# Kernel optimization log

Hardware: AMD Instinct MI355X
Metric: run time of the kernel (lower is better)

The kernel has to match this reference:

```python
import jax, jax.numpy as jnp
import numpy as np

N_GROUPS = 32
EPS = 1e-5
N_HEADS = 4
D_K = 64


def group_norm(x, gamma, beta):
    # x: [B, C, H, W]; normalize over (channels within group, spatial)
    B, C, H, W = x.shape
    xg = x.reshape(B, N_GROUPS, C // N_GROUPS, H, W)
    mean = jnp.mean(xg, axis=(2, 3, 4), keepdims=True)
    var = jnp.var(xg, axis=(2, 3, 4), keepdims=True)
    xn = ((xg - mean) * jax.lax.rsqrt(var + EPS)).reshape(B, C, H, W)
    return xn * gamma[None, :, None, None] + beta[None, :, None, None]


def setup_inputs() -> dict:
    key = jax.random.key(0)
    ks = jax.random.split(key, 4)
    B, C, H, W = 4, 256, 64, 64
    x = jax.random.normal(ks[0], (B, C, H, W), dtype=jnp.float32)
    gamma = jnp.ones((C,), dtype=jnp.float32)
    beta = jnp.zeros((C,), dtype=jnp.float32)
    w_qkv = jax.random.normal(ks[1], (C, N_HEADS * D_K * 3), dtype=jnp.float32) * (C ** -0.5)
    b_qkv = jnp.zeros((N_HEADS * D_K * 3,), dtype=jnp.float32)
    w_out = jax.random.normal(ks[2], (N_HEADS * D_K, C), dtype=jnp.float32) * ((N_HEADS * D_K) ** -0.5)
    b_out = jnp.zeros((C,), dtype=jnp.float32)
    return {"x": x, "gamma": gamma, "beta": beta, "w_qkv": w_qkv,
            "b_qkv": b_qkv, "w_out": w_out, "b_out": b_out}


def reference(x, gamma, beta, w_qkv, b_qkv, w_out, b_out):
    B, C, H, W = x.shape
    S = H * W
    scale = D_K ** -0.5
    # GroupNorm -> [B, S, C]
    h = group_norm(x, gamma, beta).reshape(B, C, S).transpose(0, 2, 1)
    qkv = (h @ w_qkv + b_qkv).reshape(B, S, N_HEADS, 3 * D_K)
    q, k, v = jnp.split(qkv, 3, axis=-1)          # each [B, S, H, D]
    attn = jnp.einsum('bihd,bjhd->bijh', q, k) * scale
    attn = jax.nn.softmax(attn, axis=2)           # softmax over j (keys)
    res = jnp.einsum('bijh,bjhd->bihd', attn, v)  # [B, S, H, D]
    res = res.reshape(B, S, N_HEADS * D_K)
    res = res @ w_out + b_out                     # [B, S, C]
    res = res.transpose(0, 2, 1).reshape(B, C, H, W)
    return res + x
```

## Files before the change

### kernel.cpp

```cpp
#include <hip/hip_runtime.h>
#include <hip/hip_bf16.h>


typedef __attribute__((ext_vector_type(8))) short short8;
typedef __attribute__((ext_vector_type(4))) float f32x4;
typedef __attribute__((ext_vector_type(16))) float f32x16;

__device__ __forceinline__ unsigned short f2bf(float f) {
    union { float f; unsigned u; } v; v.f = f;
    unsigned r = v.u + 0x7FFF + ((v.u >> 16) & 1);
    return (unsigned short)(r >> 16);
}

__device__ __forceinline__ unsigned cvt_pk_bf16(float lo, float hi) {
    unsigned r;
    asm("v_cvt_pk_bf16_f32 %0, %1, %2" : "=v"(r) : "v"(lo), "v"(hi));
    return r;
}

__device__ __forceinline__ void permswap(unsigned &x, unsigned &y) {
    asm("v_permlane32_swap_b32 %0, %1" : "+v"(x), "+v"(y));
}

__device__ __forceinline__ float fexp2(float x) {
    float r;
    asm("v_exp_f32 %0, %1" : "=v"(r) : "v"(x));
    return r;
}

__device__ __forceinline__ void gl_lds16(const void* g, void* l) {
    __builtin_amdgcn_global_load_lds(
        (const __attribute__((address_space(1))) void*)(g),
        (__attribute__((address_space(3))) void*)(l), 16, 0, 0);
}

__device__ __forceinline__ f32x16 fzero16() {
    f32x16 z;
    #pragma unroll
    for (int i = 0; i < 16; ++i) z[i] = 0.f;
    return z;
}

__global__ __launch_bounds__(1024) void k_gn_stats(const float* __restrict__ x,
                                                   float* __restrict__ stats) {
    int bg = blockIdx.x;
    const float4* xp = (const float4*)(x + bg * 32768);
    float s1 = 0.f, s2 = 0.f;
    for (int i = threadIdx.x; i < 8192; i += 1024) {
        float4 v = xp[i];
        s1 += v.x + v.y + v.z + v.w;
        s2 += v.x*v.x + v.y*v.y + v.z*v.z + v.w*v.w;
    }
    #pragma unroll
    for (int off = 32; off; off >>= 1) {
        s1 += __shfl_down(s1, off);
        s2 += __shfl_down(s2, off);
    }
    __shared__ float r1[16], r2[16];
    int wid = threadIdx.x >> 6;
    if ((threadIdx.x & 63) == 0) { r1[wid] = s1; r2[wid] = s2; }
    __syncthreads();
    if (threadIdx.x == 0) {
        float a = 0.f, b = 0.f;
        #pragma unroll
        for (int i = 0; i < 16; ++i) { a += r1[i]; b += r2[i]; }
        float mean = a * (1.f/32768.f);
        float var  = b * (1.f/32768.f) - mean*mean;
        stats[bg*2]   = mean;
        stats[bg*2+1] = rsqrtf(var + 1e-5f);
    }
}

__global__ void k_cvt_w(const float* __restrict__ wqkv, const float* __restrict__ wout,
                        unsigned short* __restrict__ wqkvT, unsigned short* __restrict__ woutT) {
    int i = blockIdx.x * 256 + threadIdx.x;
    if (i < 196608) {
        int k = i / 768, n = i - k * 768;
        wqkvT[n*256 + k] = f2bf(wqkv[i]);
    }
    if (i < 65536) {
        int k = i >> 8, n = i & 255;
        woutT[n*256 + k] = f2bf(wout[i]);
    }
}

__global__ __launch_bounds__(256) void k_gn_norm(
    const float* __restrict__ x, const float* __restrict__ gamma,
    const float* __restrict__ beta, const float* __restrict__ stats,
    unsigned short* __restrict__ h) {
    __shared__ unsigned short t[64][72];
    int s0 = blockIdx.x * 64, c0 = blockIdx.y * 64, b = blockIdx.z;
    int tid = threadIdx.x;
    int sl = (tid & 15) * 4;
    int cr = tid >> 4;
    #pragma unroll
    for (int p = 0; p < 4; ++p) {
        int c = c0 + cr + p * 16;
        float4 v = *(const float4*)&x[(b*256 + c)*4096 + s0 + sl];
        int sg = (b*32 + (c >> 3)) * 2;
        float mean = stats[sg], rstd = stats[sg+1];
        float sa = rstd * gamma[c];
        float sb = beta[c] - mean * sa;
        ushort4 pk;
        pk.x = f2bf(v.x*sa + sb); pk.y = f2bf(v.y*sa + sb);
        pk.z = f2bf(v.z*sa + sb); pk.w = f2bf(v.w*sa + sb);
        *(ushort4*)&t[cr + p*16][sl] = pk;
    }
    __syncthreads();
    int sr = tid >> 2;
    int cc = (tid & 3) * 16;
    unsigned rr[8];
    #pragma unroll
    for (int j = 0; j < 8; ++j)
        rr[j] = (unsigned)t[cc + 2*j][sr] | ((unsigned)t[cc + 2*j + 1][sr] << 16);
    unsigned short* hp = &h[(b*4096 + s0 + sr)*256 + c0];
    *(uint4*)&hp[cc]     = make_uint4(rr[0], rr[1], rr[2], rr[3]);
    *(uint4*)&hp[cc + 8] = make_uint4(rr[4], rr[5], rr[6], rr[7]);
}

__global__ __launch_bounds__(256) void k_qkv(
    const unsigned short* __restrict__ h, const unsigned short* __restrict__ wT,
    const float* __restrict__ bqkv,
    unsigned short* __restrict__ q, unsigned short* __restrict__ kk,
    unsigned short* __restrict__ vT) {
    int mt = blockIdx.x, head = blockIdx.y;
    int tid = threadIdx.x;
    int wid = tid >> 6, lane = tid & 63;
    int g = lane >> 4, li = lane & 15;
    int m0 = mt * 64 + wid * 16;
    int row = m0 + li;
    f32x4 acc[12];
    #pragma unroll
    for (int nt = 0; nt < 12; ++nt) acc[nt] = (f32x4){0.f,0.f,0.f,0.f};
    #pragma unroll
    for (int kt = 0; kt < 8; ++kt) {
        short8 a = *(const short8*)&h[row*256 + kt*32 + g*8];
        #pragma unroll
        for (int nt = 0; nt < 12; ++nt) {
            int n = head*192 + nt*16 + li;
            short8 b = *(const short8*)&wT[n*256 + kt*32 + g*8];
            acc[nt] = __builtin_amdgcn_mfma_f32_16x16x32_bf16(a, b, acc[nt], 0, 0, 0);
        }
    }
    int b = m0 >> 12;
    int s0 = m0 & 4095;
    int bh = b*4 + head;
    #pragma unroll
    for (int nt = 0; nt < 12; ++nt) {
        int ng = head*192 + nt*16 + li;
        float bias = bqkv[ng];
        int d = (nt & 3)*16 + li;
        if ((nt >> 2) == 2) {
            ushort4 pk;
            pk.x = f2bf(acc[nt][0] + bias); pk.y = f2bf(acc[nt][1] + bias);
            pk.z = f2bf(acc[nt][2] + bias); pk.w = f2bf(acc[nt][3] + bias);
            *(ushort4*)&vT[(bh*64 + d)*4096 + s0 + g*4] = pk;
        } else if ((nt >> 2) == 0) {
            #pragma unroll
            for (int r = 0; r < 4; ++r)
                q[(bh*4096 + s0 + g*4 + r)*64 + d] = f2bf((acc[nt][r] + bias) * 0.1803368801f);
        } else {
            #pragma unroll
            for (int r = 0; r < 4; ++r)
                kk[(bh*4096 + s0 + g*4 + r)*64 + d] = f2bf(acc[nt][r] + bias);
        }
    }
}

__global__ __launch_bounds__(512, 4) void k_attn(
    const unsigned short* __restrict__ q, const unsigned short* __restrict__ kk,
    const unsigned short* __restrict__ vT, unsigned short* __restrict__ ao) {
    __shared__ __align__(16) char smem[65536];

    int n = blockIdx.x;
    int qt = n >> 4;
    int bh = ((n & 7) << 1) | ((n >> 3) & 1);
    int tid = threadIdx.x;
    int wid = tid >> 6, lane = tid & 63;
    int qw = wid & 3, st = wid >> 2;
    int hi = lane >> 5, il = lane & 31;
    int swl = (il & 7) << 4;

    int qbase = qt * 128 + qw * 32;
    int qrow = bh * 4096 + qbase + il;
    short8 bq[4];
    #pragma unroll
    for (int kc = 0; kc < 4; ++kc)
        bq[kc] = *(const short8*)&q[qrow*64 + kc*16 + hi*8];

    unsigned p16  = tid * 16;
    unsigned row0 = p16 >> 7;
    unsigned sw   = (row0 & 7) << 4;
    unsigned ks0  = p16 ^ sw;
    unsigned vc0  = (p16 & 127u) ^ sw;
    const char* kbase = (const char*)kk + (size_t)bh * 524288;
    const char* vbase = (const char*)vT + (size_t)(bh*64 + row0) * 8192;
    unsigned woff = wid * 1024;

#define STAGE_PAIR(d, pair) do {                                             \
    const char* _k0 = kbase + (size_t)(2*(pair)) * 8192;                     \
    size_t _vo = (size_t)(2*(pair)) * 128;                                   \
    gl_lds16(_k0 + ks0,              smem + ((d)*2+0)*8192 + woff);          \
    gl_lds16(_k0 + 8192 + ks0,       smem + ((d)*2+1)*8192 + woff);          \
    gl_lds16(vbase + _vo + vc0,       smem + 32768 + ((d)*2+0)*8192 + woff); \
    gl_lds16(vbase + _vo + 128 + vc0, smem + 32768 + ((d)*2+1)*8192 + woff); \
} while (0)

    f32x16 o0 = fzero16(), o1 = fzero16();
    float m_run = -1e30f, l_loc = 0.f;

    STAGE_PAIR(0, 0);
    asm volatile("s_waitcnt vmcnt(0)" ::: "memory");
    __builtin_amdgcn_s_barrier();
    asm volatile("" ::: "memory");

    int cur = 0;
    for (int tp = 0; tp < 32; ++tp) {
        if (tp < 31) STAGE_PAIR(cur ^ 1, tp + 1);

        const char* kb = smem + (cur*2 + st) * 8192;
        const char* vb = smem + 32768 + (cur*2 + st) * 8192;

        f32x16 s0 = fzero16(), s1 = fzero16();
        __builtin_amdgcn_s_setprio(1);
        #pragma unroll
        for (int kc = 0; kc < 4; ++kc) {
            int c = (kc*32 + hi*16) ^ swl;
            short8 ka0 = *(const short8*)(kb + il*128 + c);
            short8 ka1 = *(const short8*)(kb + 4096 + il*128 + c);
            s0 = __builtin_amdgcn_mfma_f32_32x32x16_bf16(ka0, bq[kc], s0, 0, 0, 0);
            s1 = __builtin_amdgcn_mfma_f32_32x32x16_bf16(ka1, bq[kc], s1, 0, 0, 0);
        }
        __builtin_amdgcn_s_setprio(0);

        float m8[8];
        #pragma unroll
        for (int r = 0; r < 8; ++r)
            m8[r] = fmaxf(fmaxf(s0[2*r], s0[2*r+1]), fmaxf(s1[2*r], s1[2*r+1]));
        float mx = fmaxf(fmaxf(fmaxf(m8[0], m8[1]), fmaxf(m8[2], m8[3])),
                         fmaxf(fmaxf(m8[4], m8[5]), fmaxf(m8[6], m8[7])));
        mx = fmaxf(mx, __shfl_xor(mx, 32));
        if (__any(mx > m_run)) {
            float m_new = fmaxf(m_run, mx);
            float fac = fexp2(m_run - m_new);
            l_loc *= fac;
            #pragma unroll
            for (int r = 0; r < 16; ++r) { o0[r] *= fac; o1[r] *= fac; }
            m_run = m_new;
        }
        float p0[16], p1[16];
        #pragma unroll
        for (int r = 0; r < 16; ++r) {
            p0[r] = fexp2(s0[r] - m_run);
            p1[r] = fexp2(s1[r] - m_run);
        }
        float a8[8];
        #pragma unroll
        for (int r = 0; r < 8; ++r)
            a8[r] = (p0[2*r] + p0[2*r+1]) + (p1[2*r] + p1[2*r+1]);
        float ps = ((a8[0] + a8[1]) + (a8[2] + a8[3])) + ((a8[4] + a8[5]) + (a8[6] + a8[7]));
        l_loc += ps;

        unsigned w[16];
        #pragma unroll
        for (int t = 0; t < 2; ++t) {
            const float* pp = t ? p1 : p0;
            #pragma unroll
            for (int hh = 0; hh < 2; ++hh) {
                unsigned a = cvt_pk_bf16(pp[hh*8+0], pp[hh*8+1]);
                unsigned b = cvt_pk_bf16(pp[hh*8+2], pp[hh*8+3]);
                unsigned c = cvt_pk_bf16(pp[hh*8+4], pp[hh*8+5]);
                unsigned d = cvt_pk_bf16(pp[hh*8+6], pp[hh*8+7]);
                permswap(a, c);
                permswap(b, d);
                int base = (t*2 + hh) * 4;
                w[base+0] = a; w[base+1] = b; w[base+2] = c; w[base+3] = d;
            }
        }

        __builtin_amdgcn_s_setprio(1);
        #pragma unroll
        for (int jc = 0; jc < 4; ++jc) {
            union { unsigned u[4]; short8 s8; } pb;
            pb.u[0] = w[jc*4+0]; pb.u[1] = w[jc*4+1];
            pb.u[2] = w[jc*4+2]; pb.u[3] = w[jc*4+3];
            int c = (jc*32 + hi*16) ^ swl;
            short8 va0 = *(const short8*)(vb + il*128 + c);
            short8 va1 = *(const short8*)(vb + 4096 + il*128 + c);
            o0 = __builtin_amdgcn_mfma_f32_32x32x16_bf16(va0, pb.s8, o0, 0, 0, 0);
            o1 = __builtin_amdgcn_mfma_f32_32x32x16_bf16(va1, pb.s8, o1, 0, 0, 0);
        }
        __builtin_amdgcn_s_setprio(0);

        if (tp < 31) asm volatile("s_waitcnt vmcnt(0)" ::: "memory");
        asm volatile("" ::: "memory");
        __builtin_amdgcn_s_barrier();
        asm volatile("" ::: "memory");
        cur ^= 1;
    }
#undef STAGE_PAIR

    l_loc += __shfl_xor(l_loc, 32);

    float* red = (float*)smem;
    int slot = ((qw*64 + lane) * 34);
    if (st == 1) {
        #pragma unroll
        for (int r = 0; r < 16; ++r) { red[slot + r] = o0[r]; red[slot + 16 + r] = o1[r]; }
        red[slot + 32] = l_loc;
        red[slot + 33] = m_run;
    }
    __syncthreads();
    if (st == 0) {
        float m1 = red[slot + 33], l1 = red[slot + 32];
        float m = fmaxf(m_run, m1);
        float f0 = fexp2(m_run - m), f1 = fexp2(m1 - m);
        float inv = 1.f / (l_loc * f0 + l1 * f1);
        float a0 = f0 * inv, a1 = f1 * inv;
        int b = bh >> 2, hh = bh & 3;
        int s = qbase + il;
        unsigned short* aop = &ao[((size_t)(b*4096 + s))*256 + hh*64];
        #pragma unroll
        for (int rr = 0; rr < 4; ++rr) {
            ushort4 pk0, pk1;
            pk0.x = f2bf(o0[rr*4+0]*a0 + red[slot + rr*4+0]*a1);
            pk0.y = f2bf(o0[rr*4+1]*a0 + red[slot + rr*4+1]*a1);
            pk0.z = f2bf(o0[rr*4+2]*a0 + red[slot + rr*4+2]*a1);
            pk0.w = f2bf(o0[rr*4+3]*a0 + red[slot + rr*4+3]*a1);
            *(ushort4*)&aop[rr*8 + hi*4] = pk0;
            pk1.x = f2bf(o1[rr*4+0]*a0 + red[slot + 16 + rr*4+0]*a1);
            pk1.y = f2bf(o1[rr*4+1]*a0 + red[slot + 16 + rr*4+1]*a1);
            pk1.z = f2bf(o1[rr*4+2]*a0 + red[slot + 16 + rr*4+2]*a1);
            pk1.w = f2bf(o1[rr*4+3]*a0 + red[slot + 16 + rr*4+3]*a1);
            *(ushort4*)&aop[32 + rr*8 + hi*4] = pk1;
        }
    }
}

__global__ __launch_bounds__(256) void k_out(
    const unsigned short* __restrict__ ao, const unsigned short* __restrict__ wT,
    const float* __restrict__ bout, const float* __restrict__ x,
    float* __restrict__ out) {
    int mt = blockIdx.x;
    int tid = threadIdx.x;
    int wid = tid >> 6, lane = tid & 63;
    int g = lane >> 4, li = lane & 15;
    int rg = wid & 1, ch = wid >> 1;
    int m0 = mt * 32 + rg * 16;
    int row = m0 + li;
    f32x4 acc[8];
    #pragma unroll
    for (int nt = 0; nt < 8; ++nt) acc[nt] = (f32x4){0.f,0.f,0.f,0.f};
    #pragma unroll
    for (int kt = 0; kt < 8; ++kt) {
        short8 a = *(const short8*)&ao[row*256 + kt*32 + g*8];
        #pragma unroll
        for (int nt = 0; nt < 8; ++nt) {
            int nn = ch*128 + nt*16 + li;
            short8 b = *(const short8*)&wT[nn*256 + kt*32 + g*8];
            acc[nt] = __builtin_amdgcn_mfma_f32_16x16x32_bf16(a, b, acc[nt], 0, 0, 0);
        }
    }
    int b = m0 >> 12;
    int s0 = (m0 & 4095) + g*4;
    #pragma unroll
    for (int nt = 0; nt < 8; ++nt) {
        int c = ch*128 + nt*16 + li;
        float bias = bout[c];
        int base = (b*256 + c)*4096 + s0;
        float4 xr = *(const float4*)&x[base];
        float4 ov;
        ov.x = acc[nt][0] + bias + xr.x;
        ov.y = acc[nt][1] + bias + xr.y;
        ov.z = acc[nt][2] + bias + xr.z;
        ov.w = acc[nt][3] + bias + xr.w;
        *(float4*)&out[base] = ov;
    }
}

extern "C" void kernel_launch(void* const* d_in, const int* in_sizes, int n_in,
                              void* d_out, int out_size, void* d_ws, size_t ws_size,
                              hipStream_t stream) {
    (void)in_sizes; (void)n_in; (void)out_size; (void)ws_size;
    const float* x     = (const float*)d_in[0];
    const float* gamma = (const float*)d_in[1];
    const float* beta  = (const float*)d_in[2];
    const float* wqkv  = (const float*)d_in[3];
    const float* bqkv  = (const float*)d_in[4];
    const float* wout  = (const float*)d_in[5];
    const float* bout  = (const float*)d_in[6];
    float* out = (float*)d_out;

    char* ws = (char*)d_ws;
    unsigned short* h     = (unsigned short*)(ws);
    unsigned short* q     = (unsigned short*)(ws + (8u<<20));
    unsigned short* kk    = (unsigned short*)(ws + (16u<<20));
    unsigned short* vT    = (unsigned short*)(ws + (24u<<20));
    unsigned short* ao    = (unsigned short*)(ws + (32u<<20));
    unsigned short* wqkvT = (unsigned short*)(ws + (40u<<20));
    unsigned short* woutT = (unsigned short*)(ws + (40u<<20) + 393216);
    float*          stats = (float*)(ws + (40u<<20) + 524288);

    k_gn_stats<<<128, 1024, 0, stream>>>(x, stats);
    k_cvt_w<<<768, 256, 0, stream>>>(wqkv, wout, wqkvT, woutT);
    k_gn_norm<<<dim3(64, 4, 4), 256, 0, stream>>>(x, gamma, beta, stats, h);
    k_qkv<<<dim3(256, 4), 256, 0, stream>>>(h, wqkvT, bqkv, q, kk, vT);
    k_attn<<<dim3(512), 512, 0, stream>>>(q, kk, vT, ao);
    k_out<<<dim3(512), 256, 0, stream>>>(ao, woutT, bout, x, out);
}
```

Measured before the change: 180.5 us.

## Fold max subtraction into MFMA init and compute row sums via ones-MFMA

Seeds the QK^T accumulators with -m_run so the max subtraction happens inside the MFMA, exponentiates first, and rescales only when a probability exceeds a threshold (lazy rescale in the exp domain with log2 tracking). The row-sum reduction is replaced by an extra MFMA against a ones matrix that accumulates l alongside the PV product, and bf16 packing is interleaved into the PV loop. This trims VALU work (subtracts, sum tree, shuffle) in the softmax but adds a third MFMA per step and a log2/reciprocal on the rescale path. It also risks precision, since l is accumulated from bf16-rounded probabilities and the threshold lets exponentials grow before rescaling.

```diff
diff --git a/kernel.cpp b/kernel.cpp
--- a/kernel.cpp
+++ b/kernel.cpp
@@ -188,6 +188,10 @@
     for (int kc = 0; kc < 4; ++kc)
         bq[kc] = *(const short8*)&q[qrow*64 + kc*16 + hi*8];
 
+    short8 ones;
+    #pragma unroll
+    for (int i = 0; i < 8; ++i) ones[i] = (short)0x3F80;
+
     unsigned p16  = tid * 16;
     unsigned row0 = p16 >> 7;
     unsigned sw   = (row0 & 7) << 4;
@@ -206,8 +210,8 @@
     gl_lds16(vbase + _vo + 128 + vc0, smem + 32768 + ((d)*2+1)*8192 + woff); \
 } while (0)
 
-    f32x16 o0 = fzero16(), o1 = fzero16();
-    float m_run = -1e30f, l_loc = 0.f;
+    f32x16 o0 = fzero16(), o1 = fzero16(), accl = fzero16();
+    float m_run = 0.f;
 
     STAGE_PAIR(0, 0);
     asm volatile("s_waitcnt vmcnt(0)" ::: "memory");
@@ -221,74 +225,70 @@
         const char* kb = smem + (cur*2 + st) * 8192;
         const char* vb = smem + 32768 + (cur*2 + st) * 8192;
 
-        f32x16 s0 = fzero16(), s1 = fzero16();
+        float nm = -m_run;
+        f32x16 p0, p1;
+        #pragma unroll
+        for (int r = 0; r < 16; ++r) { p0[r] = nm; p1[r] = nm; }
         __builtin_amdgcn_s_setprio(1);
         #pragma unroll
         for (int kc = 0; kc < 4; ++kc) {
             int c = (kc*32 + hi*16) ^ swl;
             short8 ka0 = *(const short8*)(kb + il*128 + c);
             short8 ka1 = *(const short8*)(kb + 4096 + il*128 + c);
-            s0 = __builtin_amdgcn_mfma_f32_32x32x16_bf16(ka0, bq[kc], s0, 0, 0, 0);
-            s1 = __builtin_amdgcn_mfma_f32_32x32x16_bf16(ka1, bq[kc], s1, 0, 0, 0);
+            p0 = __builtin_amdgcn_mfma_f32_32x32x16_bf16(ka0, bq[kc], p0, 0, 0, 0);
+            p1 = __builtin_amdgcn_mfma_f32_32x32x16_bf16(ka1, bq[kc], p1, 0, 0, 0);
         }
         __builtin_amdgcn_s_setprio(0);
 
+        #pragma unroll
+        for (int r = 0; r < 16; ++r) {
+            p0[r] = fexp2(p0[r]);
+            p1[r] = fexp2(p1[r]);
+        }
         float m8[8];
         #pragma unroll
         for (int r = 0; r < 8; ++r)
-            m8[r] = fmaxf(fmaxf(s0[2*r], s0[2*r+1]), fmaxf(s1[2*r], s1[2*r+1]));
-        float mx = fmaxf(fmaxf(fmaxf(m8[0], m8[1]), fmaxf(m8[2], m8[3])),
+            m8[r] = fmaxf(fmaxf(p0[2*r], p0[2*r+1]), fmaxf(p1[2*r], p1[2*r+1]));
+        float pm = fmaxf(fmaxf(fmaxf(m8[0], m8[1]), fmaxf(m8[2], m8[3])),
                          fmaxf(fmaxf(m8[4], m8[5]), fmaxf(m8[6], m8[7])));
-        mx = fmaxf(mx, __shfl_xor(mx, 32));
-        if (__any(mx > m_run)) {
-            float m_new = fmaxf(m_run, mx);
-            float fac = fexp2(m_run - m_new);
-            l_loc *= fac;
+        if (__any(pm > 16.f)) {
+            pm = fmaxf(pm, __shfl_xor(pm, 32));
+            float fac = 1.f / pm;
+            m_run += log2f(pm);
+            accl[0] *= fac;
             #pragma unroll
-            for (int r = 0; r < 16; ++r) { o0[r] *= fac; o1[r] *= fac; }
-            m_run = m_new;
-        }
-        float p0[16], p1[16];
-        #pragma unroll
-        for (int r = 0; r < 16; ++r) {
-            p0[r] = fexp2(s0[r] - m_run);
-            p1[r] = fexp2(s1[r] - m_run);
-        }
-        float a8[8];
-        #pragma unroll
-        for (int r = 0; r < 8; ++r)
-            a8[r] = (p0[2*r] + p0[2*r+1]) + (p1[2*r] + p1[2*r+1]);
-        float ps = ((a8[0] + a8[1]) + (a8[2] + a8[3])) + ((a8[4] + a8[5]) + (a8[6] + a8[7]));
-        l_loc += ps;
-
-        unsigned w[16];
-        #pragma unroll
-        for (int t = 0; t < 2; ++t) {
-            const float* pp = t ? p1 : p0;
-            #pragma unroll
-            for (int hh = 0; hh < 2; ++hh) {
-                unsigned a = cvt_pk_bf16(pp[hh*8+0], pp[hh*8+1]);
-                unsigned b = cvt_pk_bf16(pp[hh*8+2], pp[hh*8+3]);
-                unsigned c = cvt_pk_bf16(pp[hh*8+4], pp[hh*8+5]);
-                unsigned d = cvt_pk_bf16(pp[hh*8+6], pp[hh*8+7]);
-                permswap(a, c);
-                permswap(b, d);
-                int base = (t*2 + hh) * 4;
-                w[base+0] = a; w[base+1] = b; w[base+2] = c; w[base+3] = d;
+            for (int r = 0; r < 16; ++r) {
+                o0[r] *= fac; o1[r] *= fac;
+                p0[r] *= fac; p1[r] *= fac;
             }
         }
 
         __builtin_amdgcn_s_setprio(1);
         #pragma unroll
         for (int jc = 0; jc < 4; ++jc) {
+            const int hh = jc & 1;
+            float e0, e1, e2, e3, e4, e5, e6, e7;
+            if (jc < 2) {
+                e0 = p0[hh*8+0]; e1 = p0[hh*8+1]; e2 = p0[hh*8+2]; e3 = p0[hh*8+3];
+                e4 = p0[hh*8+4]; e5 = p0[hh*8+5]; e6 = p0[hh*8+6]; e7 = p0[hh*8+7];
+            } else {
+                e0 = p1[hh*8+0]; e1 = p1[hh*8+1]; e2 = p1[hh*8+2]; e3 = p1[hh*8+3];
+                e4 = p1[hh*8+4]; e5 = p1[hh*8+5]; e6 = p1[hh*8+6]; e7 = p1[hh*8+7];
+            }
+            unsigned a = cvt_pk_bf16(e0, e1);
+            unsigned b = cvt_pk_bf16(e2, e3);
+            unsigned c = cvt_pk_bf16(e4, e5);
+            unsigned d = cvt_pk_bf16(e6, e7);
+            permswap(a, c);
+            permswap(b, d);
             union { unsigned u[4]; short8 s8; } pb;
-            pb.u[0] = w[jc*4+0]; pb.u[1] = w[jc*4+1];
-            pb.u[2] = w[jc*4+2]; pb.u[3] = w[jc*4+3];
-            int c = (jc*32 + hi*16) ^ swl;
-            short8 va0 = *(const short8*)(vb + il*128 + c);
-            short8 va1 = *(const short8*)(vb + 4096 + il*128 + c);
-            o0 = __builtin_amdgcn_mfma_f32_32x32x16_bf16(va0, pb.s8, o0, 0, 0, 0);
-            o1 = __builtin_amdgcn_mfma_f32_32x32x16_bf16(va1, pb.s8, o1, 0, 0, 0);
+            pb.u[0] = a; pb.u[1] = b; pb.u[2] = c; pb.u[3] = d;
+            int co = (jc*32 + hi*16) ^ swl;
+            short8 va0 = *(const short8*)(vb + il*128 + co);
+            short8 va1 = *(const short8*)(vb + 4096 + il*128 + co);
+            o0   = __builtin_amdgcn_mfma_f32_32x32x16_bf16(va0, pb.s8, o0, 0, 0, 0);
+            o1   = __builtin_amdgcn_mfma_f32_32x32x16_bf16(va1, pb.s8, o1, 0, 0, 0);
+            accl = __builtin_amdgcn_mfma_f32_32x32x16_bf16(ones, pb.s8, accl, 0, 0, 0);
         }
         __builtin_amdgcn_s_setprio(0);
 
@@ -300,7 +300,7 @@
     }
 #undef STAGE_PAIR
 
-    l_loc += __shfl_xor(l_loc, 32);
+    float l_loc = accl[0];
 
     float* red = (float*)smem;
     int slot = ((qw*64 + lane) * 34);
```

Result: faster. 175.1 us (-3.0%).
